# Performance work log

Hardware: AMD Instinct MI355X
Metric: run time of the kernel (lower is better)

The kernel has to match this reference:

```python
import jax, jax.numpy as jnp
import numpy as np

OLD = (64, 64)      # fine grid (coord_dims)
NEW = (32, 32)      # coarse grid (dims // 2)
N_ORDERS = 6        # multi-indices for order-2, 2D PDE
NUM_VAR = 12288     # pde.var_set.num_vars
NUM_EPS = 4096      # pde.var_set.num_added_eps_vars (= n constraints M)
US = 1e5            # make_AAt us
DS = 1e-5           # make_AAt ds


def setup_inputs() -> dict:
    key = jax.random.key(0)
    k = jax.random.split(key, 5)
    B = 2
    gs = OLD[0] * OLD[1]
    coeffs = jax.random.normal(k[0], (B, gs, N_ORDERS), jnp.float32)
    rhs = jax.random.normal(k[1], (B, gs), jnp.float32)
    steps_x = jax.random.uniform(k[2], (B, OLD[0] - 1), jnp.float32)
    steps_y = jax.random.uniform(k[3], (B, OLD[1] - 1), jnp.float32)
    # dense stand-in for the assembled sparse constraint matrix [B, M, N]
    A = jax.random.normal(k[4], (B, NUM_EPS, NUM_VAR + NUM_EPS), jnp.float32) * 0.01
    return {"coeffs": coeffs, "rhs": rhs, "steps_x": steps_x, "steps_y": steps_y, "A": A}


def _resize_bilinear(x, new_hw):
    # torch F.interpolate(mode='bilinear', align_corners=False) == jax.image.resize 'linear'
    return jax.image.resize(x, x.shape[:-2] + tuple(new_hw), method="linear")


def reference(coeffs, rhs, steps_x, steps_y, A):
    B = coeffs.shape[0]
    # downsample_coeffs: [B, gs, O] -> [B, O, H, W] -> bilinear -> [B, gs', O]
    c = coeffs.transpose(0, 2, 1).reshape(B, N_ORDERS, *OLD)
    c = _resize_bilinear(c, NEW).reshape(B, N_ORDERS, -1).transpose(0, 2, 1)
    # downsample_rhs
    r = _resize_bilinear(rhs.reshape(B, 1, *OLD), NEW).reshape(B, -1)
    # downsample_steps: drop last, sum adjacent pairs
    def ds_steps(s, n):
        return s[:, :-1].reshape(B, n // 2 - 1, 2).sum(axis=-1)
    sx = ds_steps(steps_x, OLD[0])
    sy = ds_steps(steps_y, OLD[1])
    # make_AAt: P_diag = [ds*1_numvar, us*1_numeps]; AAt = A Pinv A^T (batch 0); D = diag of batched A Pinv A^T
    Pinv = 1.0 / jnp.concatenate([
        jnp.full((NUM_VAR,), DS, A.dtype),
        jnp.full((NUM_EPS,), US, A.dtype),
    ])
    AAt = jnp.einsum("mn,n,kn->mk", A[0], Pinv, A[0])[None]  # [1, M, M]
    D = jnp.einsum("n,bmn->bm", Pinv, A * A)                   # [B, M]
    return (c, r, sx, sy, AAt, D)
```

## Files before the change

kernel.cpp:

```cpp
#include <hip/hip_runtime.h>
#include <cstddef>


#define NVAR 12288
#define NN   16384
#define MM   4096

typedef __bf16 bf8v __attribute__((ext_vector_type(8)));
typedef float  f4v  __attribute__((ext_vector_type(4)));
typedef float  f16v __attribute__((ext_vector_type(16)));
typedef int    i8x  __attribute__((ext_vector_type(8)));
typedef int    i4x  __attribute__((ext_vector_type(4)));
typedef unsigned short u16;
typedef unsigned char  u8;

__device__ __forceinline__ void gld_lds16(const void* g, void* l) {
  __builtin_amdgcn_global_load_lds((const __attribute__((address_space(1))) void*)g,
                                   (__attribute__((address_space(3))) void*)l,
                                   16, 0, 0);
}

__device__ __forceinline__ u16 f2bf(float x) {
  unsigned int u = __float_as_uint(x);
  u = (u + 0x7fffu + ((u >> 16) & 1u)) >> 16;
  return (u16)u;
}

__device__ __forceinline__ unsigned int f2fp4(float x) {
  const unsigned s = (__float_as_uint(x) >> 28) & 0x8u;
  const float ax = fabsf(x);
  unsigned c;
  if (ax < 1.75f)
    c = (ax < 0.75f) ? (ax < 0.25f ? 0u : 1u) : (ax < 1.25f ? 2u : 3u);
  else
    c = (ax < 3.5f) ? (ax < 2.5f ? 4u : 5u) : (ax < 5.0f ? 6u : 7u);
  return s | c;
}

__device__ __forceinline__ void make_taps(int i, float w[4], int p[4]) {
  const float rw[4] = {0.25f, 0.75f, 0.75f, 0.25f};
  float s = 0.f;
#pragma unroll
  for (int t = 0; t < 4; ++t) {
    int pp = 2 * i - 1 + t;
    bool v = (pp >= 0) && (pp < 64);
    p[t] = v ? pp : 0;
    w[t] = v ? rw[t] : 0.f;
    s += w[t];
  }
  float inv = 1.f / s;
#pragma unroll
  for (int t = 0; t < 4; ++t) w[t] *= inv;
}

__device__ __forceinline__ void pair32(int p, int& bi, int& bj) {
  int i = 0;
  while (((i + 1) * (63 - (i + 1))) / 2 <= p) ++i;
  bi = i;
  bj = i + 1 + (p - (i * (63 - i)) / 2);
}

__device__ __forceinline__ void small_ops_body(int idx,
                                               const float* __restrict__ coeffs,
                                               const float* __restrict__ rhs,
                                               const float* __restrict__ stx,
                                               const float* __restrict__ sty,
                                               float* __restrict__ out) {
  if (idx < 12288) {
    int b = idx / 6144, rem = idx % 6144;
    int pix = rem / 6, o = rem % 6;
    int yi = pix >> 5, xi = pix & 31;
    float wy[4], wx[4]; int py[4], px[4];
    make_taps(yi, wy, py);
    make_taps(xi, wx, px);
    float acc = 0.f;
#pragma unroll
    for (int dy = 0; dy < 4; ++dy) {
      float sx = 0.f;
#pragma unroll
      for (int dx = 0; dx < 4; ++dx)
        sx += wx[dx] * coeffs[((size_t)b * 4096 + py[dy] * 64 + px[dx]) * 6 + o];
      acc += wy[dy] * sx;
    }
    out[idx] = acc;
  } else if (idx < 14336) {
    int j = idx - 12288;
    int b = j >> 10, pix = j & 1023;
    int yi = pix >> 5, xi = pix & 31;
    float wy[4], wx[4]; int py[4], px[4];
    make_taps(yi, wy, py);
    make_taps(xi, wx, px);
    float acc = 0.f;
#pragma unroll
    for (int dy = 0; dy < 4; ++dy) {
      float sx = 0.f;
#pragma unroll
      for (int dx = 0; dx < 4; ++dx)
        sx += wx[dx] * rhs[(size_t)b * 4096 + py[dy] * 64 + px[dx]];
      acc += wy[dy] * sx;
    }
    out[idx] = acc;
  } else if (idx < 14460) {
    int j = idx - 14336;
    if (j < 62) {
      int b = j / 31, i = j % 31;
      out[idx] = stx[b * 63 + 2 * i] + stx[b * 63 + 2 * i + 1];
    } else {
      j -= 62;
      int b = j / 31, i = j % 31;
      out[idx] = sty[b * 63 + 2 * i] + sty[b * 63 + 2 * i + 1];
    }
  }
}

__global__ void small_ops(const float* __restrict__ coeffs,
                          const float* __restrict__ rhs,
                          const float* __restrict__ stx,
                          const float* __restrict__ sty,
                          float* __restrict__ out) {
  small_ops_body(blockIdx.x * 256 + threadIdx.x, coeffs, rhs, stx, sty, out);
}

__global__ __launch_bounds__(256)
void conv0_fused(const float* __restrict__ A, float* __restrict__ Dout,
                 u8* __restrict__ Abf,
                 const float* __restrict__ coeffs, const float* __restrict__ rhs,
                 const float* __restrict__ stx, const float* __restrict__ sty,
                 float* __restrict__ out) {
  const int t = threadIdx.x;
  if (blockIdx.x >= MM) {
    small_ops_body((blockIdx.x - MM) * 256 + t, coeffs, rhs, stx, sty, out);
    return;
  }
  const int m = blockIdx.x;
  const float PV = 1.0f / 1e-5f, PE = 1.0f / 1e5f;
  const float SV  = sqrtf(PV);
  const float SEE = sqrtf(PE) * 65536.0f;
  const float* __restrict__ row = A + (size_t)m * NN;
  float acc = 0.f;
#pragma unroll
  for (int i = 0; i < 16; ++i) {
    const int n = i * 1024 + t * 4;
    const f4v v = __builtin_nontemporal_load((const f4v*)(row + n));
    const bool isv = n < NVAR;
    const float pv = isv ? PV : PE;
    acc += pv * (v.x * v.x + v.y * v.y + v.z * v.z + v.w * v.w);
    const float s = isv ? SV : SEE;
    const unsigned pk = f2fp4(v.x * s) | (f2fp4(v.y * s) << 4) |
                        (f2fp4(v.z * s) << 8) | (f2fp4(v.w * s) << 12);
    *(u16*)(Abf + ((size_t)m * NN + n) / 2) = (u16)pk;
  }
#pragma unroll
  for (int off = 32; off > 0; off >>= 1) acc += __shfl_down(acc, off);
  __shared__ float red[4];
  if ((t & 63) == 0) red[t >> 6] = acc;
  __syncthreads();
  if (t == 0) Dout[m] = red[0] + red[1] + red[2] + red[3];
}

__global__ __launch_bounds__(256)
void mega(const u8* __restrict__ Abf, const float* __restrict__ A,
          float* __restrict__ C, float* __restrict__ Dout) {
  __shared__ __attribute__((aligned(16))) u8 ldsA[128 * 128];
  __shared__ __attribute__((aligned(16))) u8 ldsB[128 * 128];
  const int t = threadIdx.x;
  const int grp = blockIdx.x / 24, off = blockIdx.x % 24;

  if (off >= 16) {
    const int d = grp * 8 + (off - 16);
    const float PV = 1.0f / 1e-5f, PE = 1.0f / 1e5f;
    float* redf = (float*)ldsA;
#pragma unroll
    for (int r8 = 0; r8 < 8; ++r8) {
      const float* __restrict__ row = A + ((size_t)MM + d * 8 + r8) * NN;
      float acc = 0.f;
#pragma unroll
      for (int i = 0; i < 16; ++i) {
        const int n = i * 1024 + t * 4;
        const f4v v = __builtin_nontemporal_load((const f4v*)(row + n));
        const float pv = (n < NVAR) ? PV : PE;
        acc += pv * (v.x * v.x + v.y * v.y + v.z * v.z + v.w * v.w);
      }
#pragma unroll
      for (int o = 32; o > 0; o >>= 1) acc += __shfl_down(acc, o);
      if ((t & 63) == 0) redf[r8 * 4 + (t >> 6)] = acc;
    }
    __syncthreads();
    if (t < 8)
      Dout[MM + d * 8 + t] = redf[t * 4] + redf[t * 4 + 1] +
                             redf[t * 4 + 2] + redf[t * 4 + 3];
    return;
  }

  const int g = grp * 16 + off;
  int bi, bj, ktBeg, ktEnd;
  bool mirror;
  if (g < 32) {
    bi = bj = g; ktBeg = 0; ktEnd = 64; mirror = false;
  } else {
    const int e0 = g - 32;
    const int kid = (e0 & 7) * 124 + (e0 >> 3);
    pair32(kid >> 1, bi, bj);
    const int half = kid & 1;
    ktBeg = half * 32; ktEnd = ktBeg + 32;
    mirror = (half == 0);
  }

  const int lane = t & 63;
  const int wave = t >> 6;
  const int wr = (wave >> 1) * 64;
  const int wc = (wave & 1) * 64;
  const int pc = lane & 31;
  const int kh = lane >> 5;

  f16v acc[2][2];
#pragma unroll
  for (int i = 0; i < 2; ++i)
#pragma unroll
    for (int j = 0; j < 2; ++j)
#pragma unroll
      for (int r = 0; r < 16; ++r) acc[i][j][r] = 0.f;

  const int srow = t >> 3;
  const int hs = (t & 7) ^ (srow & 7);
  const size_t rA = (size_t)bi * 128 + srow;
  const size_t rB = (size_t)bj * 128 + srow;

  for (int kt = ktBeg; kt < ktEnd; ++kt) {
    const size_t kbB = (size_t)kt * 128;
#pragma unroll
    for (int i = 0; i < 4; ++i) {
      gld_lds16(Abf + (rA + i * 32) * 8192 + kbB + hs * 16,
                &ldsA[t * 16 + i * 4096]);
      gld_lds16(Abf + (rB + i * 32) * 8192 + kbB + hs * 16,
                &ldsB[t * 16 + i * 4096]);
    }
    __syncthreads();
    const int sc = (kt < 48) ? 127 : 111;
#pragma unroll
    for (int kk = 0; kk < 4; ++kk) {
      const int H = kk * 2 + kh;
      i8x a[2], bb[2];
#pragma unroll
      for (int fi = 0; fi < 2; ++fi) {
        int r = wr + fi * 32 + pc;
        i4x va = *(const i4x*)&ldsA[r * 128 + ((H ^ (r & 7)) << 4)];
        a[fi] = i8x{va.x, va.y, va.z, va.w, 0, 0, 0, 0};
        r = wc + fi * 32 + pc;
        i4x vb = *(const i4x*)&ldsB[r * 128 + ((H ^ (r & 7)) << 4)];
        bb[fi] = i8x{vb.x, vb.y, vb.z, vb.w, 0, 0, 0, 0};
      }
#pragma unroll
      for (int i = 0; i < 2; ++i)
#pragma unroll
        for (int j = 0; j < 2; ++j)
          acc[i][j] = __builtin_amdgcn_mfma_scale_f32_32x32x64_f8f6f4(
              a[i], bb[j], acc[i][j], 4, 4, 0, sc, 0, sc);
    }
    __syncthreads();
  }

  const int rowBase = (mirror ? bj : bi) * 128;
  const int colBase = (mirror ? bi : bj) * 128;
#pragma unroll
  for (int i = 0; i < 2; ++i)
#pragma unroll
    for (int j = 0; j < 2; ++j)
#pragma unroll
      for (int reg = 0; reg < 16; ++reg) {
        const int crow = (reg & 3) + 8 * (reg >> 2) + 4 * kh;
        const int gr = rowBase + wr + i * 32 + crow;
        const int gc = colBase + wc + j * 32 + pc;
        C[(size_t)gr * MM + gc] = acc[i][j][reg];
      }
}

__global__ __launch_bounds__(256)
void reduce_fused(float* __restrict__ C, const float* __restrict__ D0) {
  if (blockIdx.x >= 496) {
    const int m = (blockIdx.x - 496) * 256 + threadIdx.x;
    C[(size_t)m * MM + m] = D0[m];
    return;
  }
  int bi, bj;
  pair32(blockIdx.x, bi, bj);
  const int t = threadIdx.x;
  __shared__ float S0[64][68], S1[64][68];
  const size_t upBase = (size_t)bi * 128 * MM + bj * 128;
  const size_t loBase = (size_t)bj * 128 * MM + bi * 128;

#pragma unroll
  for (int q = 0; q < 2; ++q) {
    f4v s[4];
#pragma unroll
    for (int k = 0; k < 4; ++k) {
      const int idx = t + k * 256;
      const int r = idx >> 4, c4 = idx & 15;
      const size_t o = (size_t)(q * 64 + r) * MM + q * 64 + c4 * 4;
      s[k] = *(const f4v*)(C + upBase + o) + *(const f4v*)(C + loBase + o);
      S0[r][c4 * 4 + 0] = s[k].x; S0[r][c4 * 4 + 1] = s[k].y;
      S0[r][c4 * 4 + 2] = s[k].z; S0[r][c4 * 4 + 3] = s[k].w;
    }
    __syncthreads();
#pragma unroll
    for (int k = 0; k < 4; ++k) {
      const int idx = t + k * 256;
      const int r = idx >> 4, c4 = idx & 15;
      *(f4v*)(C + upBase + (size_t)(q * 64 + r) * MM + q * 64 + c4 * 4) = s[k];
    }
#pragma unroll
    for (int k = 0; k < 4; ++k) {
      const int idx = t + k * 256;
      const int R = idx >> 4, r4 = idx & 15;
      f4v w;
      w.x = S0[r4 * 4 + 0][R]; w.y = S0[r4 * 4 + 1][R];
      w.z = S0[r4 * 4 + 2][R]; w.w = S0[r4 * 4 + 3][R];
      *(f4v*)(C + loBase + (size_t)(q * 64 + R) * MM + q * 64 + r4 * 4) = w;
    }
    __syncthreads();
  }

  f4v s01[4], s10[4];
#pragma unroll
  for (int k = 0; k < 4; ++k) {
    const int idx = t + k * 256;
    const int r = idx >> 4, c4 = idx & 15;
    const size_t o01 = (size_t)r * MM + 64 + c4 * 4;
    const size_t o10 = (size_t)(64 + r) * MM + c4 * 4;
    s01[k] = *(const f4v*)(C + upBase + o01) + *(const f4v*)(C + loBase + o01);
    s10[k] = *(const f4v*)(C + upBase + o10) + *(const f4v*)(C + loBase + o10);
    S0[r][c4 * 4 + 0] = s01[k].x; S0[r][c4 * 4 + 1] = s01[k].y;
    S0[r][c4 * 4 + 2] = s01[k].z; S0[r][c4 * 4 + 3] = s01[k].w;
    S1[r][c4 * 4 + 0] = s10[k].x; S1[r][c4 * 4 + 1] = s10[k].y;
    S1[r][c4 * 4 + 2] = s10[k].z; S1[r][c4 * 4 + 3] = s10[k].w;
  }
  __syncthreads();
#pragma unroll
  for (int k = 0; k < 4; ++k) {
    const int idx = t + k * 256;
    const int r = idx >> 4, c4 = idx & 15;
    *(f4v*)(C + upBase + (size_t)r * MM + 64 + c4 * 4) = s01[k];
    *(f4v*)(C + upBase + (size_t)(64 + r) * MM + c4 * 4) = s10[k];
  }
#pragma unroll
  for (int k = 0; k < 4; ++k) {
    const int idx = t + k * 256;
    const int R = idx >> 4, r4 = idx & 15;
    f4v w;
    w.x = S0[r4 * 4 + 0][R]; w.y = S0[r4 * 4 + 1][R];
    w.z = S0[r4 * 4 + 2][R]; w.w = S0[r4 * 4 + 3][R];
    *(f4v*)(C + loBase + (size_t)(64 + R) * MM + r4 * 4) = w;
    f4v v;
    v.x = S1[r4 * 4 + 0][R]; v.y = S1[r4 * 4 + 1][R];
    v.z = S1[r4 * 4 + 2][R]; v.w = S1[r4 * 4 + 3][R];
    *(f4v*)(C + loBase + (size_t)R * MM + 64 + r4 * 4) = v;
  }
}

__global__ void write_diag(float* __restrict__ C, const float* __restrict__ D0) {
  const int m = blockIdx.x * 256 + threadIdx.x;
  C[(size_t)m * MM + m] = D0[m];
}

__global__ __launch_bounds__(256)
void d_only(const float* __restrict__ A, float* __restrict__ Dout) {
  const int m = blockIdx.x, b = blockIdx.y;
  const int t = threadIdx.x;
  const float PV = 1.0f / 1e-5f, PE = 1.0f / 1e5f;
  const float* __restrict__ row = A + ((size_t)b * MM + m) * NN;
  float acc = 0.f;
#pragma unroll
  for (int i = 0; i < 16; ++i) {
    const int n = i * 1024 + t * 4;
    const f4v v = __builtin_nontemporal_load((const f4v*)(row + n));
    const float pv = (n < NVAR) ? PV : PE;
    acc += pv * (v.x * v.x + v.y * v.y + v.z * v.z + v.w * v.w);
  }
#pragma unroll
  for (int off = 32; off > 0; off >>= 1) acc += __shfl_down(acc, off);
  __shared__ float red[4];
  if ((t & 63) == 0) red[t >> 6] = acc;
  __syncthreads();
  if (t == 0) Dout[(size_t)b * MM + m] = red[0] + red[1] + red[2] + red[3];
}

__global__ __launch_bounds__(256)
void reduce_sum_fb(float* __restrict__ C) {
  int bi, bj;
  pair32(blockIdx.x, bi, bj);
  const int t = threadIdx.x;
#pragma unroll
  for (int k = 0; k < 16; ++k) {
    const int idx = t + k * 256;
    const int r = idx >> 5, c4 = idx & 31;
    float* up = C + (size_t)(bi * 128 + r) * MM + bj * 128 + c4 * 4;
    const float* lo = C + (size_t)(bj * 128 + r) * MM + bi * 128 + c4 * 4;
    f4v u = *(const f4v*)up;
    u += *(const f4v*)lo;
    *(f4v*)up = u;
  }
}

__global__ __launch_bounds__(256)
void reduce_mirror_fb(float* __restrict__ C) {
  int bi, bj;
  pair32(blockIdx.x, bi, bj);
  const int t = threadIdx.x;
  __shared__ float S[64][132];
#pragma unroll
  for (int s = 0; s < 2; ++s) {
#pragma unroll
    for (int k = 0; k < 8; ++k) {
      const int idx = t + k * 256;
      const int r = idx >> 5, c4 = idx & 31;
      const f4v v = *(const f4v*)(C + (size_t)(bi * 128 + s * 64 + r) * MM +
                                  bj * 128 + c4 * 4);
      S[r][c4 * 4 + 0] = v.x; S[r][c4 * 4 + 1] = v.y;
      S[r][c4 * 4 + 2] = v.z; S[r][c4 * 4 + 3] = v.w;
    }
    __syncthreads();
#pragma unroll
    for (int k = 0; k < 8; ++k) {
      const int idx = t + k * 256;
      const int c = idx >> 4, r4 = idx & 15;
      f4v w;
      w.x = S[r4 * 4 + 0][c]; w.y = S[r4 * 4 + 1][c];
      w.z = S[r4 * 4 + 2][c]; w.w = S[r4 * 4 + 3][c];
      *(f4v*)(C + (size_t)(bj * 128 + c) * MM + bi * 128 + s * 64 + r4 * 4) = w;
    }
    __syncthreads();
  }
}

__global__ __launch_bounds__(256, 4)
void old_gemm(const float* __restrict__ A0, float* __restrict__ C) {
  const int id = blockIdx.x;
  int bi, bj, ktBeg, ktEnd;
  bool mirror;
  if (id < 32) { bi = bj = id; ktBeg = 0; ktEnd = 256; mirror = false; }
  else {
    const int e0 = id - 32;
    const int kid = (e0 & 7) * 124 + (e0 >> 3);
    pair32(kid >> 1, bi, bj);
    const int half = kid & 1;
    ktBeg = half * 128; ktEnd = ktBeg + 128;
    mirror = (half == 0);
  }
  __shared__ u16 ldsA[128 * 64];
  __shared__ u16 ldsB[128 * 64];
  const int t = threadIdx.x, lane = t & 63, wave = t >> 6;
  const int wr = (wave >> 1) * 64, wc = (wave & 1) * 64;
  f4v acc[4][4];
#pragma unroll
  for (int i = 0; i < 4; ++i)
#pragma unroll
    for (int j = 0; j < 4; ++j) acc[i][j] = f4v{0.f, 0.f, 0.f, 0.f};
  const int srow = t >> 3;
  const int scol = (((t & 7) ^ (srow & 7)) * 8);
  const size_t rA = (size_t)bi * 128 + srow, rB = (size_t)bj * 128 + srow;
  const int ldse = t * 8;
  const float SV = sqrtf(1.0f / 1e-5f), SE = sqrtf(1.0f / 1e5f);
  const int q = lane >> 4, p = lane & 15;
  const int csw0 = ((0 * 4 + q) ^ (p & 7)) * 8;
  const int csw1 = ((1 * 4 + q) ^ (p & 7)) * 8;
  for (int kt = ktBeg; kt < ktEnd; ++kt) {
    const int n = kt * 64 + scol;
    const float s = (n < NVAR) ? SV : SE;
#pragma unroll
    for (int i = 0; i < 4; ++i) {
      const float* ga = A0 + (rA + i * 32) * NN + n;
      const float* gb = A0 + (rB + i * 32) * NN + n;
      const f4v a0 = ((const f4v*)ga)[0], a1 = ((const f4v*)ga)[1];
      const f4v b0 = ((const f4v*)gb)[0], b1 = ((const f4v*)gb)[1];
      u16* dA = &ldsA[i * 2048 + ldse];
      u16* dB = &ldsB[i * 2048 + ldse];
      dA[0] = f2bf(a0.x * s); dA[1] = f2bf(a0.y * s);
      dA[2] = f2bf(a0.z * s); dA[3] = f2bf(a0.w * s);
      dA[4] = f2bf(a1.x * s); dA[5] = f2bf(a1.y * s);
      dA[6] = f2bf(a1.z * s); dA[7] = f2bf(a1.w * s);
      dB[0] = f2bf(b0.x * s); dB[1] = f2bf(b0.y * s);
      dB[2] = f2bf(b0.z * s); dB[3] = f2bf(b0.w * s);
      dB[4] = f2bf(b1.x * s); dB[5] = f2bf(b1.y * s);
      dB[6] = f2bf(b1.z * s); dB[7] = f2bf(b1.w * s);
    }
    __syncthreads();
#pragma unroll
    for (int kk = 0; kk < 2; ++kk) {
      const int co = kk ? csw1 : csw0;
      bf8v af[4], bfr[4];
#pragma unroll
      for (int i = 0; i < 4; ++i)
        af[i] = *(const bf8v*)&ldsA[(wr + i * 16 + p) * 64 + co];
#pragma unroll
      for (int j = 0; j < 4; ++j)
        bfr[j] = *(const bf8v*)&ldsB[(wc + j * 16 + p) * 64 + co];
#pragma unroll
      for (int i = 0; i < 4; ++i)
#pragma unroll
        for (int j = 0; j < 4; ++j)
          acc[i][j] = __builtin_amdgcn_mfma_f32_16x16x32_bf16(af[i], bfr[j],
                                                              acc[i][j], 0, 0, 0);
    }
    __syncthreads();
  }
  const int rowBase = (mirror ? bj : bi) * 128;
  const int colBase = (mirror ? bi : bj) * 128;
#pragma unroll
  for (int i = 0; i < 4; ++i)
#pragma unroll
    for (int j = 0; j < 4; ++j)
#pragma unroll
      for (int r = 0; r < 4; ++r)
        C[(size_t)(rowBase + wr + i * 16 + q * 4 + r) * MM +
          colBase + wc + j * 16 + p] = acc[i][j][r];
}

extern "C" void kernel_launch(void* const* d_in, const int* in_sizes, int n_in,
                              void* d_out, int out_size, void* d_ws,
                              size_t ws_size, hipStream_t stream) {
  const float* coeffs = (const float*)d_in[0];
  const float* rhs    = (const float*)d_in[1];
  const float* stx    = (const float*)d_in[2];
  const float* sty    = (const float*)d_in[3];
  const float* A      = (const float*)d_in[4];

  float* out    = (float*)d_out;
  float* outAAt = out + 14460;
  float* outD   = out + 16791676;

  const size_t need = (size_t)MM * NN / 2;
  const int useWs = (ws_size >= need) ? 1 : 0;
  u8* Abf = (u8*)d_ws;

  if (useWs) {
    conv0_fused<<<dim3(MM + 57), dim3(256), 0, stream>>>(
        A, outD, Abf, coeffs, rhs, stx, sty, out);
    mega<<<dim3(1536), dim3(256), 0, stream>>>(Abf, A, outAAt, outD);
    reduce_fused<<<dim3(512), dim3(256), 0, stream>>>(outAAt, outD);
  } else {
    small_ops<<<dim3(57), dim3(256), 0, stream>>>(coeffs, rhs, stx, sty, out);
    d_only<<<dim3(MM, 2), dim3(256), 0, stream>>>(A, outD);
    old_gemm<<<dim3(1024), dim3(256), 0, stream>>>(A, outAAt);
    reduce_sum_fb<<<dim3(496), dim3(256), 0, stream>>>(outAAt);
    reduce_mirror_fb<<<dim3(496), dim3(256), 0, stream>>>(outAAt);
    write_diag<<<dim3(16), dim3(256), 0, stream>>>(outAAt, outD);
  }
}
```

Measured before the change: 230.4 us.

## Interleave batch-1 diagonal reduction loads into GEMM K-loop blocks

Removes the dedicated D-reduction blocks from the mega kernel. Each GEMM block now also computes the batch-1 diagonal for 4 rows of A, issuing the fp32 row loads between GEMM K-steps so the streaming traffic overlaps with MFMA work. The grid shrinks from 1536 to 1024 blocks. The risks are higher register pressure, and diagonal blocks doing 64 K-steps while off-diagonal blocks do 32, which makes per-block D work uneven.

After: 240.8 us. +4.5%, slower.

```diff
diff --git a/kernel.cpp b/kernel.cpp
--- a/kernel.cpp
+++ b/kernel.cpp
@@ -164,45 +164,19 @@
   __shared__ __attribute__((aligned(16))) u8 ldsA[128 * 128];
   __shared__ __attribute__((aligned(16))) u8 ldsB[128 * 128];
   const int t = threadIdx.x;
-  const int grp = blockIdx.x / 24, off = blockIdx.x % 24;
-
-  if (off >= 16) {
-    const int d = grp * 8 + (off - 16);
-    const float PV = 1.0f / 1e-5f, PE = 1.0f / 1e5f;
-    float* redf = (float*)ldsA;
-#pragma unroll
-    for (int r8 = 0; r8 < 8; ++r8) {
-      const float* __restrict__ row = A + ((size_t)MM + d * 8 + r8) * NN;
-      float acc = 0.f;
-#pragma unroll
-      for (int i = 0; i < 16; ++i) {
-        const int n = i * 1024 + t * 4;
-        const f4v v = __builtin_nontemporal_load((const f4v*)(row + n));
-        const float pv = (n < NVAR) ? PV : PE;
-        acc += pv * (v.x * v.x + v.y * v.y + v.z * v.z + v.w * v.w);
-      }
-#pragma unroll
-      for (int o = 32; o > 0; o >>= 1) acc += __shfl_down(acc, o);
-      if ((t & 63) == 0) redf[r8 * 4 + (t >> 6)] = acc;
-    }
-    __syncthreads();
-    if (t < 8)
-      Dout[MM + d * 8 + t] = redf[t * 4] + redf[t * 4 + 1] +
-                             redf[t * 4 + 2] + redf[t * 4 + 3];
-    return;
-  }
-
-  const int g = grp * 16 + off;
-  int bi, bj, ktBeg, ktEnd;
-  bool mirror;
+  const int g = blockIdx.x;
+
+  int bi, bj;
+  int half = 0;
+  bool diag, mirror;
   if (g < 32) {
-    bi = bj = g; ktBeg = 0; ktEnd = 64; mirror = false;
+    bi = bj = g; diag = true; mirror = false;
   } else {
     const int e0 = g - 32;
     const int kid = (e0 & 7) * 124 + (e0 >> 3);
     pair32(kid >> 1, bi, bj);
-    const int half = kid & 1;
-    ktBeg = half * 32; ktEnd = ktBeg + 32;
+    half = kid & 1;
+    diag = false;
     mirror = (half == 0);
   }
 
@@ -226,7 +200,7 @@
   const size_t rA = (size_t)bi * 128 + srow;
   const size_t rB = (size_t)bj * 128 + srow;
 
-  for (int kt = ktBeg; kt < ktEnd; ++kt) {
+  auto GSTEP = [&](int kt) {
     const size_t kbB = (size_t)kt * 128;
 #pragma unroll
     for (int i = 0; i < 4; ++i) {
@@ -258,7 +232,57 @@
               a[i], bb[j], acc[i][j], 4, 4, 0, sc, 0, sc);
     }
     __syncthreads();
-  }
+  };
+
+  const float PV = 1.0f / 1e-5f, PE = 1.0f / 1e5f;
+  const f4v* __restrict__ Ab1 =
+      (const f4v*)(A + (size_t)MM * NN + (size_t)g * 4 * NN);
+  float dacc[4];
+
+  if (diag) {
+#pragma unroll
+    for (int r4 = 0; r4 < 4; ++r4) {
+      const f4v* __restrict__ dRow = Ab1 + (size_t)r4 * 4096;
+      float da = 0.f;
+      for (int s16 = 0; s16 < 16; ++s16) {
+        const f4v dv = __builtin_nontemporal_load(dRow + s16 * 256 + t);
+        GSTEP(r4 * 16 + s16);
+        const float pv = (s16 < 12) ? PV : PE;
+        da += pv * (dv.x * dv.x + dv.y * dv.y + dv.z * dv.z + dv.w * dv.w);
+      }
+      dacc[r4] = da;
+    }
+  } else {
+    const int ktBeg = half * 32;
+#pragma unroll
+    for (int r4 = 0; r4 < 4; ++r4) {
+      const f4v* __restrict__ dRow = Ab1 + (size_t)r4 * 4096;
+      float da = 0.f;
+      for (int s8 = 0; s8 < 8; ++s8) {
+        const f4v dv0 = __builtin_nontemporal_load(dRow + s8 * 512 + t * 2);
+        const f4v dv1 = __builtin_nontemporal_load(dRow + s8 * 512 + t * 2 + 1);
+        GSTEP(ktBeg + r4 * 8 + s8);
+        const float pv = (s8 < 6) ? PV : PE;
+        da += pv * (dv0.x * dv0.x + dv0.y * dv0.y + dv0.z * dv0.z +
+                    dv0.w * dv0.w + dv1.x * dv1.x + dv1.y * dv1.y +
+                    dv1.z * dv1.z + dv1.w * dv1.w);
+      }
+      dacc[r4] = da;
+    }
+  }
+
+  float* dred = (float*)ldsA;
+#pragma unroll
+  for (int r4 = 0; r4 < 4; ++r4) {
+    float v = dacc[r4];
+#pragma unroll
+    for (int o = 32; o > 0; o >>= 1) v += __shfl_down(v, o);
+    if (lane == 0) dred[r4 * 4 + wave] = v;
+  }
+  __syncthreads();
+  if (t < 4)
+    Dout[MM + g * 4 + t] =
+        dred[t * 4 + 0] + dred[t * 4 + 1] + dred[t * 4 + 2] + dred[t * 4 + 3];
 
   const int rowBase = (mirror ? bj : bi) * 128;
   const int colBase = (mirror ? bi : bj) * 128;
@@ -535,7 +559,7 @@
   if (useWs) {
     conv0_fused<<<dim3(MM + 57), dim3(256), 0, stream>>>(
         A, outD, Abf, coeffs, rhs, stx, sty, out);
-    mega<<<dim3(1536), dim3(256), 0, stream>>>(Abf, A, outAAt, outD);
+    mega<<<dim3(1024), dim3(256), 0, stream>>>(Abf, A, outAAt, outD);
     reduce_fused<<<dim3(512), dim3(256), 0, stream>>>(outAAt, outD);
   } else {
     small_ops<<<dim3(57), dim3(256), 0, stream>>>(coeffs, rhs, stx, sty, out);
```
